# Optimization experiments

Measured on AMD Instinct MI355X. Metric: run time of the kernel, lower is better.

Reference implementation:

```python
import jax, jax.numpy as jnp
import numpy as np

V, H, B, S = 32000, 512, 128, 64

def setup_inputs() -> dict:
    key = jax.random.key(0)
    ks = jax.random.split(key, 16)
    sc = 0.02
    return {
        "input_ids": jax.random.randint(ks[0], (B,), 0, V),
        "h0": jax.random.normal(ks[1], (1, B, H), jnp.float32),
        "c0": jax.random.normal(ks[2], (1, B, H), jnp.float32),
        "encoder_outputs": jax.random.normal(ks[3], (B, S, H), jnp.float32),
        "emb": jax.random.normal(ks[4], (V, H), jnp.float32) * sc,
        "attn_W": jax.random.normal(ks[5], (H, 2 * H), jnp.float32) * sc,
        "attn_b": jnp.zeros((H,), jnp.float32),
        "v": jax.random.uniform(ks[6], (H,), jnp.float32),
        "W_ih": jax.random.normal(ks[7], (4 * H, 2 * H), jnp.float32) * sc,
        "W_hh": jax.random.normal(ks[8], (4 * H, H), jnp.float32) * sc,
        "b_ih": jnp.zeros((4 * H,), jnp.float32),
        "b_hh": jnp.zeros((4 * H,), jnp.float32),
        "fc_W": jax.random.normal(ks[9], (V, H), jnp.float32) * sc,
        "fc_b": jnp.zeros((V,), jnp.float32),
    }

def reference(input_ids, h0, c0, encoder_outputs, emb, attn_W, attn_b, v,
              W_ih, W_hh, b_ih, b_hh, fc_W, fc_b):
    # Embedding lookup: [B, H]
    embedded = emb[input_ids]
    h = h0[0]  # top-layer hidden state [B, H]
    c = c0[0]
    # Bahdanau attention over encoder outputs [B, S, H]
    h_rep = jnp.broadcast_to(h[:, None, :], encoder_outputs.shape)
    cat = jnp.concatenate([h_rep, encoder_outputs], axis=-1)  # [B, S, 2H]
    energy = jnp.tanh(jnp.einsum('bsd,hd->bsh', cat, attn_W) + attn_b)
    scores = jnp.einsum('bsh,h->bs', energy, v)
    attn_weights = jax.nn.softmax(scores, axis=1)  # [B, S]
    context = jnp.einsum('bs,bsh->bh', attn_weights, encoder_outputs)
    # Single LSTM cell step (PyTorch gate order i, f, g, o)
    rnn_in = jnp.concatenate([embedded, context], axis=-1)  # [B, 2H]
    gates = rnn_in @ W_ih.T + b_ih + h @ W_hh.T + b_hh  # [B, 4H]
    i, f, g, o = jnp.split(gates, 4, axis=-1)
    c_new = jax.nn.sigmoid(f) * c + jax.nn.sigmoid(i) * jnp.tanh(g)
    h_new = jax.nn.sigmoid(o) * jnp.tanh(c_new)
    prediction = h_new @ fc_W.T + fc_b  # [B, V]
    return prediction, h_new[None], c_new[None]
```

## Files before the change

kernel.cpp:

```cpp
#include <hip/hip_runtime.h>

typedef __bf16 bf16;
typedef __bf16 bf16x8 __attribute__((ext_vector_type(8)));
typedef float f32x4 __attribute__((ext_vector_type(4)));

#define VOCAB 32000
#define HID 512
#define BATCH 128
#define SEQ 64

__device__ inline bf16x8 cvt8(float4 a, float4 b) {
  bf16x8 r;
  r[0] = (bf16)a.x; r[1] = (bf16)a.y; r[2] = (bf16)a.z; r[3] = (bf16)a.w;
  r[4] = (bf16)b.x; r[5] = (bf16)b.y; r[6] = (bf16)b.z; r[7] = (bf16)b.w;
  return r;
}

__device__ inline float fast_tanh(float x) {
  x = fminf(fmaxf(x, -15.f), 15.f);
  float e = __expf(2.f * x);
  return (e - 1.f) / (e + 1.f);
}
__device__ inline float fast_sig(float x) {
  return 1.f / (1.f + __expf(-x));
}

__global__ __launch_bounds__(512) void k_pack(
    const float* __restrict__ attn_W, bf16* __restrict__ Wp) {
  int gid = blockIdx.x * 512 + threadIdx.x;
  int hh = gid >> 7;
  int kc8 = gid & 127;
  const float* src = attn_W + (size_t)hh * 1024 + kc8 * 8;
  bf16x8 v = cvt8(((const float4*)src)[0], ((const float4*)src)[1]);
  int kchunk = kc8 >> 2, klane = kc8 & 3;
  int ntile = hh >> 4, nlane = hh & 15;
  int lane = klane * 16 + nlane;
  *(bf16x8*)(Wp + ((size_t)(kchunk * 32 + ntile) * 64 + lane) * 8) = v;
}

__global__ __launch_bounds__(512) void k_attn(
    const float* __restrict__ enc, const bf16* __restrict__ Wp,
    const float* __restrict__ attn_b, const float* __restrict__ vvec,
    const float* __restrict__ emb, const int* __restrict__ ids,
    const float* __restrict__ h0, bf16* __restrict__ Acat,
    float* __restrict__ gates_ws) {
  __shared__ char smem[65536];
  __shared__ bf16 h0s[512];
  bf16* encA = (bf16*)smem;
  float* spart = (float*)smem;
  float* wgt = (float*)(smem + 2048);
  float* ctxp = (float*)(smem + 2304);

  int b = blockIdx.x, tid = threadIdx.x;
  int w = tid >> 6, lane = tid & 63;
  int l15 = lane & 15, lq = lane >> 4;
  const float* encb = enc + (size_t)b * SEQ * HID;

  {
    int gid = b * 512 + tid;
    float4 z = {0.f, 0.f, 0.f, 0.f};
    ((float4*)gates_ws)[gid] = z;
  }

  h0s[tid] = (bf16)h0[b * 512 + tid];

#pragma unroll
  for (int i = 0; i < 8; ++i) {
    int cl = tid + i * 512;
    int row = cl >> 6;
    int c = cl & 63;
    int phys = c ^ (row & 7);
    const float4* src = (const float4*)(encb + row * 512 + c * 8);
    bf16x8 v = cvt8(src[0], src[1]);
    *(bf16x8*)(encA + row * 512 + phys * 8) = v;
  }
  __syncthreads();

  f32x4 acc[4][4];
  f32x4 acc_e1[4];
#pragma unroll
  for (int mt = 0; mt < 4; ++mt)
#pragma unroll
    for (int jn = 0; jn < 4; ++jn) acc[mt][jn] = (f32x4)0.f;
#pragma unroll
  for (int jn = 0; jn < 4; ++jn) acc_e1[jn] = (f32x4)0.f;

#pragma unroll 4
  for (int kc = 0; kc < 16; ++kc) {
    bf16x8 af = *(const bf16x8*)(h0s + kc * 32 + lq * 8);
#pragma unroll
    for (int jn = 0; jn < 4; ++jn) {
      int nt = w * 4 + jn;
      bf16x8 bfr = *(const bf16x8*)(Wp + ((size_t)(kc * 32 + nt) * 64 + lane) * 8);
      acc_e1[jn] = __builtin_amdgcn_mfma_f32_16x16x32_bf16(af, bfr, acc_e1[jn], 0, 0, 0);
    }
  }

#pragma unroll 2
  for (int kc = 16; kc < 32; ++kc) {
    bf16x8 bfr[4], af[4];
#pragma unroll
    for (int jn = 0; jn < 4; ++jn) {
      int nt = w * 4 + jn;
      bfr[jn] = *(const bf16x8*)(Wp + ((size_t)(kc * 32 + nt) * 64 + lane) * 8);
    }
#pragma unroll
    for (int mt = 0; mt < 4; ++mt) {
      int row = mt * 16 + l15;
      int c = (kc - 16) * 4 + lq;
      int phys = c ^ (row & 7);
      af[mt] = *(const bf16x8*)(encA + row * 512 + phys * 8);
    }
#pragma unroll
    for (int mt = 0; mt < 4; ++mt)
#pragma unroll
      for (int jn = 0; jn < 4; ++jn)
        acc[mt][jn] = __builtin_amdgcn_mfma_f32_16x16x32_bf16(
            af[mt], bfr[jn], acc[mt][jn], 0, 0, 0);
  }
  __syncthreads();

  float p[4][4];
#pragma unroll
  for (int mt = 0; mt < 4; ++mt)
#pragma unroll
    for (int r = 0; r < 4; ++r) p[mt][r] = 0.f;
#pragma unroll
  for (int jn = 0; jn < 4; ++jn) {
    int h = (w * 4 + jn) * 16 + l15;
    float bias = attn_b[h];
    float vv = vvec[h];
#pragma unroll
    for (int mt = 0; mt < 4; ++mt)
#pragma unroll
      for (int r = 0; r < 4; ++r)
        p[mt][r] += vv * fast_tanh(acc[mt][jn][r] + acc_e1[jn][r] + bias);
  }
#pragma unroll
  for (int mt = 0; mt < 4; ++mt)
#pragma unroll
    for (int r = 0; r < 4; ++r) {
      float x = p[mt][r];
      x += __shfl_xor(x, 1);
      x += __shfl_xor(x, 2);
      x += __shfl_xor(x, 4);
      x += __shfl_xor(x, 8);
      p[mt][r] = x;
    }
  if (l15 == 0) {
#pragma unroll
    for (int mt = 0; mt < 4; ++mt)
#pragma unroll
      for (int r = 0; r < 4; ++r) {
        int s = mt * 16 + lq * 4 + r;
        spart[w * 64 + s] = p[mt][r];
      }
  }
  __syncthreads();

  if (tid < 64) {
    float sc = 0.f;
#pragma unroll
    for (int ww = 0; ww < 8; ++ww) sc += spart[ww * 64 + tid];
    float mx = sc;
    for (int m = 32; m; m >>= 1) mx = fmaxf(mx, __shfl_xor(mx, m));
    float e = __expf(sc - mx);
    float sm = e;
    for (int m = 32; m; m >>= 1) sm += __shfl_xor(sm, m);
    wgt[tid] = e / sm;
  }
  __syncthreads();

  {
    int hc = tid & 63, sg = tid >> 6;
    float a8[8];
#pragma unroll
    for (int j = 0; j < 8; ++j) a8[j] = 0.f;
    for (int s = sg * 8; s < sg * 8 + 8; ++s) {
      float wv = wgt[s];
      const float4* src = (const float4*)(encb + s * 512 + hc * 8);
      float4 x0 = src[0], x1 = src[1];
      a8[0] += wv * x0.x; a8[1] += wv * x0.y; a8[2] += wv * x0.z; a8[3] += wv * x0.w;
      a8[4] += wv * x1.x; a8[5] += wv * x1.y; a8[6] += wv * x1.z; a8[7] += wv * x1.w;
    }
#pragma unroll
    for (int j = 0; j < 8; ++j) ctxp[sg * 512 + hc * 8 + j] = a8[j];
  }
  __syncthreads();

  {
    int h = tid;
    float c = 0.f;
#pragma unroll
    for (int g = 0; g < 8; ++g) c += ctxp[g * 512 + h];
    int id = ids[b];
    Acat[(size_t)b * 1536 + h] = (bf16)emb[(size_t)id * 512 + h];
    Acat[(size_t)b * 1536 + 512 + h] = (bf16)c;
    Acat[(size_t)b * 1536 + 1024 + h] = (bf16)h0[b * 512 + h];
  }
}

__global__ __launch_bounds__(512) void k_gates(
    const bf16* __restrict__ Acat, const float* __restrict__ W_ih,
    const float* __restrict__ W_hh, float* __restrict__ gates_ws) {
  int nb = blockIdx.x, ks = blockIdx.y;
  int tid = threadIdx.x, w = tid >> 6, lane = tid & 63;
  int l15 = lane & 15, lq = lane >> 4;
  int wm = w >> 1, wn = w & 1;

  f32x4 acc[2][2];
#pragma unroll
  for (int i = 0; i < 2; ++i)
#pragma unroll
    for (int j = 0; j < 2; ++j) acc[i][j] = (f32x4)0.f;

#pragma unroll 2
  for (int kt = 0; kt < 8; ++kt) {
    int kglob = ks * 256 + kt * 32;
    int ko = kglob + lq * 8;
    bf16x8 bfr[2], af[2];
#pragma unroll
    for (int jn = 0; jn < 2; ++jn) {
      int row = nb * 64 + (wn * 2 + jn) * 16 + l15;
      const float4* p = (kglob < 1024)
          ? (const float4*)(W_ih + (size_t)row * 1024 + ko)
          : (const float4*)(W_hh + (size_t)row * 512 + (ko - 1024));
      bfr[jn] = cvt8(p[0], p[1]);
    }
#pragma unroll
    for (int mi = 0; mi < 2; ++mi) {
      int m = (wm * 2 + mi) * 16 + l15;
      af[mi] = *(const bf16x8*)(Acat + (size_t)m * 1536 + ko);
    }
#pragma unroll
    for (int mi = 0; mi < 2; ++mi)
#pragma unroll
      for (int jn = 0; jn < 2; ++jn)
        acc[mi][jn] = __builtin_amdgcn_mfma_f32_16x16x32_bf16(
            af[mi], bfr[jn], acc[mi][jn], 0, 0, 0);
  }
#pragma unroll
  for (int mi = 0; mi < 2; ++mi)
#pragma unroll
    for (int jn = 0; jn < 2; ++jn)
#pragma unroll
      for (int rr = 0; rr < 4; ++rr) {
        int bb = (wm * 2 + mi) * 16 + lq * 4 + rr;
        int n = nb * 64 + (wn * 2 + jn) * 16 + l15;
        atomicAdd(&gates_ws[(size_t)bb * 2048 + n], acc[mi][jn][rr]);
      }
}

__global__ __launch_bounds__(512) void k_cell(
    const float* __restrict__ gates_ws, const float* __restrict__ b_ih,
    const float* __restrict__ b_hh, const float* __restrict__ c0,
    float* __restrict__ out, bf16* __restrict__ hnewb) {
  int idx = blockIdx.x * 512 + threadIdx.x;
  int b = idx >> 9, h = idx & 511;
  const float* g = gates_ws + (size_t)b * 2048;
  float iv = g[h] + b_ih[h] + b_hh[h];
  float fv = g[512 + h] + b_ih[512 + h] + b_hh[512 + h];
  float gv = g[1024 + h] + b_ih[1024 + h] + b_hh[1024 + h];
  float ov = g[1536 + h] + b_ih[1536 + h] + b_hh[1536 + h];
  float cn = fast_sig(fv) * c0[idx] + fast_sig(iv) * fast_tanh(gv);
  float hn = fast_sig(ov) * fast_tanh(cn);
  out[4096000 + idx] = hn;
  out[4096000 + 65536 + idx] = cn;
  hnewb[idx] = (bf16)hn;
}

__global__ __launch_bounds__(512) void k_fc(
    const bf16* __restrict__ hnewb, const float* __restrict__ fc_W,
    const float* __restrict__ fc_b, float* __restrict__ out) {
  int vb = blockIdx.x * 64;
  int tid = threadIdx.x, w = tid >> 6, lane = tid & 63;
  int l15 = lane & 15, lq = lane >> 4;
  int wm = w >> 1, wn = w & 1;

  f32x4 acc[2][2];
#pragma unroll
  for (int i = 0; i < 2; ++i)
#pragma unroll
    for (int j = 0; j < 2; ++j) acc[i][j] = (f32x4)0.f;

  const float* b0 = fc_W + (size_t)(vb + (wn * 2 + 0) * 16 + l15) * 512 + lq * 8;
  const float* b1 = fc_W + (size_t)(vb + (wn * 2 + 1) * 16 + l15) * 512 + lq * 8;
  const bf16* a0 = hnewb + (size_t)((wm * 2 + 0) * 16 + l15) * 512 + lq * 8;
  const bf16* a1 = hnewb + (size_t)((wm * 2 + 1) * 16 + l15) * 512 + lq * 8;

#pragma unroll 4
  for (int kt = 0; kt < 16; ++kt) {
    int ko = kt * 32;
    bf16x8 bfr[2], af[2];
    {
      const float4* p = (const float4*)(b0 + ko);
      bfr[0] = cvt8(p[0], p[1]);
    }
    {
      const float4* p = (const float4*)(b1 + ko);
      bfr[1] = cvt8(p[0], p[1]);
    }
    af[0] = *(const bf16x8*)(a0 + ko);
    af[1] = *(const bf16x8*)(a1 + ko);
#pragma unroll
    for (int mi = 0; mi < 2; ++mi)
#pragma unroll
      for (int jn = 0; jn < 2; ++jn)
        acc[mi][jn] = __builtin_amdgcn_mfma_f32_16x16x32_bf16(
            af[mi], bfr[jn], acc[mi][jn], 0, 0, 0);
  }

#pragma unroll
  for (int mi = 0; mi < 2; ++mi)
#pragma unroll
    for (int jn = 0; jn < 2; ++jn) {
      int vv = vb + (wn * 2 + jn) * 16 + l15;
      float bias = fc_b[vv];
#pragma unroll
      for (int rr = 0; rr < 4; ++rr) {
        int bb = (wm * 2 + mi) * 16 + lq * 4 + rr;
        out[(size_t)bb * 32000 + vv] = acc[mi][jn][rr] + bias;
      }
    }
}

extern "C" void kernel_launch(void* const* d_in, const int* in_sizes, int n_in,
                              void* d_out, int out_size, void* d_ws,
                              size_t ws_size, hipStream_t stream) {
  const int* ids = (const int*)d_in[0];
  const float* h0 = (const float*)d_in[1];
  const float* c0 = (const float*)d_in[2];
  const float* enc = (const float*)d_in[3];
  const float* emb = (const float*)d_in[4];
  const float* attn_W = (const float*)d_in[5];
  const float* attn_b = (const float*)d_in[6];
  const float* vvec = (const float*)d_in[7];
  const float* W_ih = (const float*)d_in[8];
  const float* W_hh = (const float*)d_in[9];
  const float* b_ih = (const float*)d_in[10];
  const float* b_hh = (const float*)d_in[11];
  const float* fc_W = (const float*)d_in[12];
  const float* fc_b = (const float*)d_in[13];
  float* out = (float*)d_out;
  char* ws = (char*)d_ws;

  bf16* Wp = (bf16*)ws;
  bf16* Acat = (bf16*)(ws + 1048576);
  bf16* hnewb = (bf16*)(ws + 1441792);
  float* gates = (float*)(ws + 1572864);

  k_pack<<<128, 512, 0, stream>>>(attn_W, Wp);
  k_attn<<<128, 512, 0, stream>>>(enc, Wp, attn_b, vvec, emb, ids, h0, Acat, gates);
  k_gates<<<dim3(32, 6), 512, 0, stream>>>(Acat, W_ih, W_hh, gates);
  k_cell<<<128, 512, 0, stream>>>(gates, b_ih, b_hh, c0, out, hnewb);
  k_fc<<<500, 512, 0, stream>>>(hnewb, fc_W, fc_b, out);
}
```

Baseline: 254.9 us.

## Stage weight tiles in swizzled LDS for gates and fc GEMMs, halve fc tile

In both the LSTM gate GEMM and the output projection, each block now loads its fp32 weight tile once with coalesced float4 reads, converts it to bf16 and stores it in LDS using an XOR swizzle. The MFMA loop then reads B fragments from LDS instead of issuing strided global loads per wave. Before, warps in the same block re-read and re-converted overlapping weight rows. The fc kernel also drops to a 32-column tile with 1000 blocks for more parallelism. This adds a barrier, LDS use and a serial load phase before any compute begins.

```diff
diff --git a/kernel.cpp b/kernel.cpp
--- a/kernel.cpp
+++ b/kernel.cpp
@@ -204,28 +204,41 @@
     const bf16* __restrict__ Acat, const float* __restrict__ W_ih,
     const float* __restrict__ W_hh, float* __restrict__ gates_ws) {
   int nb = blockIdx.x, ks = blockIdx.y;
+  __shared__ bf16 Wl[64 * 256];
   int tid = threadIdx.x, w = tid >> 6, lane = tid & 63;
   int l15 = lane & 15, lq = lane >> 4;
   int wm = w >> 1, wn = w & 1;
 
+#pragma unroll
+  for (int i = 0; i < 4; ++i) {
+    int g = i * 512 + tid;
+    int row = g >> 5, c = g & 31;
+    int kcol = ks * 256 + c * 8;
+    int grow = nb * 64 + row;
+    const float4* p = (ks < 4)
+        ? (const float4*)(W_ih + (size_t)grow * 1024 + kcol)
+        : (const float4*)(W_hh + (size_t)grow * 512 + (kcol - 1024));
+    int phys = c ^ (row & 7);
+    *(bf16x8*)(Wl + row * 256 + phys * 8) = cvt8(p[0], p[1]);
+  }
+  __syncthreads();
+
   f32x4 acc[2][2];
 #pragma unroll
   for (int i = 0; i < 2; ++i)
 #pragma unroll
     for (int j = 0; j < 2; ++j) acc[i][j] = (f32x4)0.f;
 
-#pragma unroll 2
+#pragma unroll 4
   for (int kt = 0; kt < 8; ++kt) {
-    int kglob = ks * 256 + kt * 32;
-    int ko = kglob + lq * 8;
+    int ko = ks * 256 + kt * 32 + lq * 8;
     bf16x8 bfr[2], af[2];
 #pragma unroll
     for (int jn = 0; jn < 2; ++jn) {
-      int row = nb * 64 + (wn * 2 + jn) * 16 + l15;
-      const float4* p = (kglob < 1024)
-          ? (const float4*)(W_ih + (size_t)row * 1024 + ko)
-          : (const float4*)(W_hh + (size_t)row * 512 + (ko - 1024));
-      bfr[jn] = cvt8(p[0], p[1]);
+      int row = (wn * 2 + jn) * 16 + l15;
+      int c = kt * 4 + lq;
+      int phys = c ^ (row & 7);
+      bfr[jn] = *(const bf16x8*)(Wl + row * 256 + phys * 8);
     }
 #pragma unroll
     for (int mi = 0; mi < 2; ++mi) {
@@ -272,55 +285,49 @@
 __global__ __launch_bounds__(512) void k_fc(
     const bf16* __restrict__ hnewb, const float* __restrict__ fc_W,
     const float* __restrict__ fc_b, float* __restrict__ out) {
-  int vb = blockIdx.x * 64;
+  int vb = blockIdx.x * 32;
+  __shared__ bf16 Wl[32 * 512];
   int tid = threadIdx.x, w = tid >> 6, lane = tid & 63;
   int l15 = lane & 15, lq = lane >> 4;
   int wm = w >> 1, wn = w & 1;
 
-  f32x4 acc[2][2];
-#pragma unroll
-  for (int i = 0; i < 2; ++i)
-#pragma unroll
-    for (int j = 0; j < 2; ++j) acc[i][j] = (f32x4)0.f;
-
-  const float* b0 = fc_W + (size_t)(vb + (wn * 2 + 0) * 16 + l15) * 512 + lq * 8;
-  const float* b1 = fc_W + (size_t)(vb + (wn * 2 + 1) * 16 + l15) * 512 + lq * 8;
+#pragma unroll
+  for (int i = 0; i < 4; ++i) {
+    int g = i * 512 + tid;
+    int row = g >> 6, c = g & 63;
+    const float4* p = (const float4*)(fc_W + (size_t)(vb + row) * 512 + c * 8);
+    int phys = c ^ (row & 7);
+    *(bf16x8*)(Wl + row * 512 + phys * 8) = cvt8(p[0], p[1]);
+  }
+  __syncthreads();
+
+  f32x4 acc[2];
+  acc[0] = (f32x4)0.f;
+  acc[1] = (f32x4)0.f;
+
   const bf16* a0 = hnewb + (size_t)((wm * 2 + 0) * 16 + l15) * 512 + lq * 8;
   const bf16* a1 = hnewb + (size_t)((wm * 2 + 1) * 16 + l15) * 512 + lq * 8;
+  int browbase = wn * 16 + l15;
 
 #pragma unroll 4
   for (int kt = 0; kt < 16; ++kt) {
-    int ko = kt * 32;
-    bf16x8 bfr[2], af[2];
-    {
-      const float4* p = (const float4*)(b0 + ko);
-      bfr[0] = cvt8(p[0], p[1]);
-    }
-    {
-      const float4* p = (const float4*)(b1 + ko);
-      bfr[1] = cvt8(p[0], p[1]);
-    }
-    af[0] = *(const bf16x8*)(a0 + ko);
-    af[1] = *(const bf16x8*)(a1 + ko);
-#pragma unroll
-    for (int mi = 0; mi < 2; ++mi)
-#pragma unroll
-      for (int jn = 0; jn < 2; ++jn)
-        acc[mi][jn] = __builtin_amdgcn_mfma_f32_16x16x32_bf16(
-            af[mi], bfr[jn], acc[mi][jn], 0, 0, 0);
-  }
-
+    int c = kt * 4 + lq;
+    int phys = c ^ (browbase & 7);
+    bf16x8 bfr = *(const bf16x8*)(Wl + browbase * 512 + phys * 8);
+    bf16x8 af0 = *(const bf16x8*)(a0 + kt * 32);
+    bf16x8 af1 = *(const bf16x8*)(a1 + kt * 32);
+    acc[0] = __builtin_amdgcn_mfma_f32_16x16x32_bf16(af0, bfr, acc[0], 0, 0, 0);
+    acc[1] = __builtin_amdgcn_mfma_f32_16x16x32_bf16(af1, bfr, acc[1], 0, 0, 0);
+  }
+
+  int vv = vb + wn * 16 + l15;
+  float bias = fc_b[vv];
 #pragma unroll
   for (int mi = 0; mi < 2; ++mi)
 #pragma unroll
-    for (int jn = 0; jn < 2; ++jn) {
-      int vv = vb + (wn * 2 + jn) * 16 + l15;
-      float bias = fc_b[vv];
-#pragma unroll
-      for (int rr = 0; rr < 4; ++rr) {
-        int bb = (wm * 2 + mi) * 16 + lq * 4 + rr;
-        out[(size_t)bb * 32000 + vv] = acc[mi][jn][rr] + bias;
-      }
+    for (int rr = 0; rr < 4; ++rr) {
+      int bb = (wm * 2 + mi) * 16 + lq * 4 + rr;
+      out[(size_t)bb * 32000 + vv] = acc[mi][rr] + bias;
     }
 }
 
@@ -353,5 +360,5 @@
   k_attn<<<128, 512, 0, stream>>>(enc, Wp, attn_b, vvec, emb, ids, h0, Acat, gates);
   k_gates<<<dim3(32, 6), 512, 0, stream>>>(Acat, W_ih, W_hh, gates);
   k_cell<<<128, 512, 0, stream>>>(gates, b_ih, b_hh, c0, out, hnewb);
-  k_fc<<<500, 512, 0, stream>>>(hnewb, fc_W, fc_b, out);
-}
+  k_fc<<<1000, 512, 0, stream>>>(hnewb, fc_W, fc_b, out);
+}
```

New measurement: 244.8 us. 1.04x faster.
